# Kernel optimization log

Measured on AMD Instinct MI355X. Metric: run time of the kernel, lower is better.

Reference implementation:

```python
import jax, jax.numpy as jnp
import numpy as np
import math

N_EMBD = 512
N_BRANCH = 4
BLOCK = 2048
B, T = 2, 2048


def make_rope_tables(dim, max_len):
    inv_freq = 1.0 / (10000.0 ** (np.arange(0, dim, 2, dtype=np.float32) / dim))
    t = np.arange(max_len, dtype=np.float32)
    freqs = np.einsum('i,j->ij', t, inv_freq)  # [max_len, dim/2]
    return jnp.asarray(np.cos(freqs)), jnp.asarray(np.sin(freqs))


def apply_rope(xq, cos, sin):
    # xq: [..., T, C]; cos/sin: [T, C/2]
    x1 = xq[..., 0::2]
    x2 = xq[..., 1::2]
    y1 = x1 * cos - x2 * sin
    y2 = x1 * sin + x2 * cos
    return jnp.stack((y1, y2), axis=-1).reshape(xq.shape)


def setup_inputs() -> dict:
    key = jax.random.key(0)
    ks = jax.random.split(key, 6)
    C, NB = N_EMBD, N_BRANCH
    s = 1.0 / math.sqrt(C)
    a = jax.random.normal(ks[0], (B, T, C), jnp.float32)
    x = jax.random.normal(ks[1], (B, T, C), jnp.float32)
    Wq = jax.random.normal(ks[2], (C, C * NB), jnp.float32) * s
    Wk = jax.random.normal(ks[3], (C, C), jnp.float32) * s
    Wv = jax.random.normal(ks[4], (C, C * NB), jnp.float32) * s
    Wo = jax.random.normal(ks[5], (C, C), jnp.float32) * s
    cos, sin = make_rope_tables(C, BLOCK)
    return {"a": a, "x": x, "Wq": Wq, "Wk": Wk, "Wv": Wv, "Wo": Wo,
            "cos": cos, "sin": sin}


def reference(a, x, Wq, Wk, Wv, Wo, cos, sin):
    Bb, Tt, C = x.shape
    NB = Wq.shape[1] // C
    cos_t = cos[:Tt]
    sin_t = sin[:Tt]

    q = (a @ Wq).reshape(Bb, Tt, NB, C).transpose(0, 2, 1, 3)  # [B,NB,T,C]
    v = (a @ Wv).reshape(Bb, Tt, NB, C).transpose(0, 2, 1, 3)  # [B,NB,T,C]
    k = (x @ Wk)[:, None, :, :]                                # [B,1,T,C]

    q = apply_rope(q, cos_t, sin_t)
    k = apply_rope(k, cos_t, sin_t)

    att = jnp.einsum('bntc,bosc->bnts', q, k) / math.sqrt(C)   # [B,NB,T,T]
    causal = jnp.tril(jnp.ones((Tt, Tt), bool))                # [T,T]
    att_m = jnp.where(causal, att, -jnp.inf)

    # softmax over branch axis; mask is identical across branches, so compute
    # on unmasked logits and zero-out masked positions (== nan_to_num of
    # softmax over fully -inf columns)
    soft_probs = jnp.where(causal, jax.nn.softmax(att, axis=1), 0.0)

    max_val = jnp.max(soft_probs, axis=1, keepdims=True)
    hard_mask = jax.lax.stop_gradient((soft_probs == max_val).astype(att.dtype))
    route_mask = jax.lax.stop_gradient(hard_mask - soft_probs) + soft_probs

    att_max = jnp.max(att_m, axis=1)                           # [B,T,T]
    attn_probs = jax.nn.softmax(att_max, axis=-1)              # [B,T,T]

    combined = attn_probs[:, None, :, :] * route_mask          # [B,NB,T,T]
    y = jnp.einsum('bnts,bnsc->btc', combined, v)              # [B,T,C]
    return y @ Wo
```

## Files before the change

### kernel.cpp

```cpp
#include <hip/hip_runtime.h>
#include <math.h>


#define B_ 2
#define T_ 2048
#define C_ 512
#define NB_ 4
#define C2_ 1024

typedef unsigned short u16;
typedef unsigned char u8;
using short8 = __attribute__((ext_vector_type(8))) short;
using bf16x8 = __attribute__((ext_vector_type(8))) __bf16;
using f32x4  = __attribute__((ext_vector_type(4))) float;

__device__ __forceinline__ float bf2f(u16 u) {
  union { unsigned int i; float f; } v; v.i = ((unsigned int)u) << 16; return v.f;
}
__device__ __forceinline__ u16 f2bf(float f) {
  union { float f; unsigned int i; } v; v.f = f;
  unsigned int u = v.i;
  return (u16)((u + 0x7fffu + ((u >> 16) & 1u)) >> 16);
}
__device__ __forceinline__ f32x4 mfma16x16x32(short8 a, short8 b, f32x4 c) {
  return __builtin_amdgcn_mfma_f32_16x16x32_bf16(
      __builtin_bit_cast(bf16x8, a), __builtin_bit_cast(bf16x8, b), c, 0, 0, 0);
}
__device__ __forceinline__ void split8(const float* s, uint4& hi, uint4& lo) {
  u16 h[8], l[8];
#pragma unroll
  for (int j = 0; j < 8; ++j) {
    h[j] = f2bf(s[j]);
    l[j] = f2bf(s[j] - bf2f(h[j]));
  }
  hi.x = h[0] | ((unsigned)h[1] << 16); hi.y = h[2] | ((unsigned)h[3] << 16);
  hi.z = h[4] | ((unsigned)h[5] << 16); hi.w = h[6] | ((unsigned)h[7] << 16);
  lo.x = l[0] | ((unsigned)l[1] << 16); lo.y = l[2] | ((unsigned)l[3] << 16);
  lo.z = l[4] | ((unsigned)l[5] << 16); lo.w = l[6] | ((unsigned)l[7] << 16);
}
__device__ __forceinline__ int swz(int row) { return ((row >> 1) & 3) << 3; }

template <int MODE>
__global__ __launch_bounds__(256) void gemm_qk(const float* __restrict__ A,
                                               const float* __restrict__ W,
                                               u16* __restrict__ out,
                                               const float* __restrict__ cosT,
                                               const float* __restrict__ sinT,
                                               const int N, const int K) {
  __shared__ u16 Ah[64][32], Al[64][32];
  __shared__ u16 Bh[64][32], Bl[64][32];
  const int tid = threadIdx.x;
  const int wave = tid >> 6, lane = tid & 63;
  const int m0 = blockIdx.y << 6, n0 = blockIdx.x << 6;
  const f32x4 zero = {0.f, 0.f, 0.f, 0.f};
  f32x4 acc[4] = {zero, zero, zero, zero};
  const int srow = tid >> 2, koff = ((tid & 3) << 3) ^ swz(tid >> 2);
  const int lrow = lane & 15, lk = ((lane >> 4) << 3) ^ swz(lane & 15);
  for (int kk = 0; kk < K; kk += 32) {
    const int kg = (tid & 3) << 3;
    float av[8];
    *(float4*)(av) = *(const float4*)(&A[(size_t)(m0 + srow) * K + kk + kg]);
    *(float4*)(av + 4) =
        *(const float4*)(&A[(size_t)(m0 + srow) * K + kk + kg + 4]);
    uint4 hi, lo;
    split8(av, hi, lo);
    *(uint4*)(&Ah[srow][koff]) = hi;
    *(uint4*)(&Al[srow][koff]) = lo;
    float wv[8];
#pragma unroll
    for (int j = 0; j < 8; ++j)
      wv[j] = W[(size_t)(kk + kg + j) * N + n0 + srow];
    split8(wv, hi, lo);
    *(uint4*)(&Bh[srow][koff]) = hi;
    *(uint4*)(&Bl[srow][koff]) = lo;
    __syncthreads();
    short8 ah = *(const short8*)(&Ah[(wave << 4) + lrow][lk]);
    short8 al = *(const short8*)(&Al[(wave << 4) + lrow][lk]);
#pragma unroll
    for (int ns = 0; ns < 4; ++ns) {
      short8 bh = *(const short8*)(&Bh[(ns << 4) + lrow][lk]);
      short8 bl = *(const short8*)(&Bl[(ns << 4) + lrow][lk]);
      acc[ns] = mfma16x16x32(ah, bh, acc[ns]);
      acc[ns] = mfma16x16x32(al, bh, acc[ns]);
      acc[ns] = mfma16x16x32(ah, bl, acc[ns]);
    }
    __syncthreads();
  }
  const int r0 = m0 + (wave << 4) + ((lane >> 4) << 2);
  const int cb = n0 + (lane & 15);
#pragma unroll
  for (int ns = 0; ns < 4; ++ns) {
#pragma unroll
    for (int r = 0; r < 4; ++r) {
      const int rg = r0 + r;
      const int cg = cb + (ns << 4);
      float v = acc[ns][r];
      float pv = __shfl_xor(v, 1);
      const int t = rg & (T_ - 1);
      const int c = (MODE == 1) ? (cg & (C_ - 1)) : cg;
      const int i = c >> 1;
      const float cf = cosT[(t << 8) + i];
      const float sf = sinT[(t << 8) + i];
      float x1 = (lane & 1) ? pv : v;
      float x2 = (lane & 1) ? v : pv;
      float y = (lane & 1) ? (x1 * sf + x2 * cf) : (x1 * cf - x2 * sf);
      if (MODE == 1) y *= 0.044194173824159216f;
      const u16 hi = f2bf(y);
      const u16 lo = f2bf(y - bf2f(hi));
      size_t rowoff;
      if (MODE == 1) {
        const int b = rg >> 11, n = cg >> 9;
        rowoff = ((size_t)((b * NB_ + n) * T_ + t)) * C2_;
      } else {
        rowoff = (size_t)rg * C2_;
      }
      out[rowoff + c] = hi;
      out[rowoff + C_ + c] = lo;
    }
  }
}

template <int AF32, int OF32>
__global__ __launch_bounds__(256) void gemm_hi(const void* __restrict__ Ap,
                                               const float* __restrict__ W,
                                               void* __restrict__ outp,
                                               const int N, const int K) {
  __shared__ u16 As[64][32];
  __shared__ u16 Bs[64][32];
  const int tid = threadIdx.x;
  const int wave = tid >> 6, lane = tid & 63;
  const int m0 = blockIdx.y << 6, n0 = blockIdx.x << 6;
  const f32x4 zero = {0.f, 0.f, 0.f, 0.f};
  f32x4 acc[4] = {zero, zero, zero, zero};
  const int srow = tid >> 2, koff = ((tid & 3) << 3) ^ swz(tid >> 2);
  const int lrow = lane & 15, lk = ((lane >> 4) << 3) ^ swz(lane & 15);
  for (int kk = 0; kk < K; kk += 32) {
    const int kg = (tid & 3) << 3;
    if (AF32) {
      const float* A = (const float*)Ap;
      float av[8];
      *(float4*)(av) = *(const float4*)(&A[(size_t)(m0 + srow) * K + kk + kg]);
      *(float4*)(av + 4) =
          *(const float4*)(&A[(size_t)(m0 + srow) * K + kk + kg + 4]);
      uint4 hi;
      hi.x = f2bf(av[0]) | ((unsigned)f2bf(av[1]) << 16);
      hi.y = f2bf(av[2]) | ((unsigned)f2bf(av[3]) << 16);
      hi.z = f2bf(av[4]) | ((unsigned)f2bf(av[5]) << 16);
      hi.w = f2bf(av[6]) | ((unsigned)f2bf(av[7]) << 16);
      *(uint4*)(&As[srow][koff]) = hi;
    } else {
      const u16* A = (const u16*)Ap;
      *(uint4*)(&As[srow][koff]) =
          *(const uint4*)(&A[(size_t)(m0 + srow) * K + kk + kg]);
    }
    uint4 hi;
    {
      float w[8];
#pragma unroll
      for (int j = 0; j < 8; ++j)
        w[j] = W[(size_t)(kk + kg + j) * N + n0 + srow];
      hi.x = f2bf(w[0]) | ((unsigned)f2bf(w[1]) << 16);
      hi.y = f2bf(w[2]) | ((unsigned)f2bf(w[3]) << 16);
      hi.z = f2bf(w[4]) | ((unsigned)f2bf(w[5]) << 16);
      hi.w = f2bf(w[6]) | ((unsigned)f2bf(w[7]) << 16);
    }
    *(uint4*)(&Bs[srow][koff]) = hi;
    __syncthreads();
    short8 af = *(const short8*)(&As[(wave << 4) + lrow][lk]);
#pragma unroll
    for (int ns = 0; ns < 4; ++ns) {
      short8 bf = *(const short8*)(&Bs[(ns << 4) + lrow][lk]);
      acc[ns] = mfma16x16x32(af, bf, acc[ns]);
    }
    __syncthreads();
  }
  const int r0 = m0 + (wave << 4) + ((lane >> 4) << 2);
  const int cb = n0 + (lane & 15);
#pragma unroll
  for (int ns = 0; ns < 4; ++ns) {
#pragma unroll
    for (int r = 0; r < 4; ++r) {
      const size_t idx = (size_t)(r0 + r) * N + cb + (ns << 4);
      if (OF32) ((float*)outp)[idx] = acc[ns][r];
      else ((u16*)outp)[idx] = f2bf(acc[ns][r]);
    }
  }
}

__global__ __launch_bounds__(256) void transpose_v_k(const u16* __restrict__ Vraw,
                                                     u16* __restrict__ VT) {
  const int bid = blockIdx.x;
  const int ct = bid & 7;
  const int ttile = (bid >> 3) & 31;
  const int n = (bid >> 8) & 3;
  const int b = bid >> 10;
  __shared__ u16 tile[64][68];
  const int tid = threadIdx.x;
  const int rr = tid >> 4;
  const int cc = (tid & 15) << 2;
  const int t0 = ttile << 6, c0 = ct << 6;
#pragma unroll
  for (int it = 0; it < 4; ++it) {
    const int r = (it << 4) + rr;
    *(ushort4*)(&tile[r][cc]) = *(const ushort4*)(
        &Vraw[((size_t)((b << 11) + t0 + r)) * (NB_ * C_) + n * C_ + c0 + cc]);
  }
  __syncthreads();
#pragma unroll
  for (int it = 0; it < 4; ++it) {
    const int c = (it << 4) + rr;
    ushort4 w;
    w.x = tile[cc + 0][c]; w.y = tile[cc + 1][c];
    w.z = tile[cc + 2][c]; w.w = tile[cc + 3][c];
    *(ushort4*)(&VT[((size_t)((b * NB_ + n) * C_ + c0 + c)) * T_ + t0 + cc]) = w;
  }
}

__global__ __launch_bounds__(256) void scores_k(const u16* __restrict__ Qcat,
                                                const u16* __restrict__ Kcat,
                                                u16* __restrict__ Mout,
                                                u8* __restrict__ Mask) {
  const int tri = ((blockIdx.x & 7) * 66) + (blockIdx.x >> 3);
  int tt = (int)((sqrtf(8.f * (float)tri + 1.f) - 1.f) * 0.5f);
  while ((tt + 1) * (tt + 2) / 2 <= tri) ++tt;
  while (tt * (tt + 1) / 2 > tri) --tt;
  const int ss = tri - tt * (tt + 1) / 2;
  const int b = blockIdx.y;
  __shared__ u16 Qh[NB_][64][32], Ql[NB_][64][32];
  __shared__ u16 Kh[64][32], Kl[64][32];
  const int tid = threadIdx.x;
  const int wave = tid >> 6, lane = tid & 63;
  const int t0 = tt << 6, s0 = ss << 6;
  const f32x4 zero = {0.f, 0.f, 0.f, 0.f};
  f32x4 acc[NB_][4];
  for (int n = 0; n < NB_; ++n)
    for (int j = 0; j < 4; ++j) acc[n][j] = zero;
  const int srow = tid >> 2, koff = ((tid & 3) << 3) ^ swz(tid >> 2);
  const int lrow = lane & 15, lk = ((lane >> 4) << 3) ^ swz(lane & 15);
  const int kg = (tid & 3) << 3;
  for (int kk = 0; kk < C_; kk += 32) {
#pragma unroll
    for (int n = 0; n < NB_; ++n) {
      const size_t qb =
          ((size_t)((b * NB_ + n) * T_ + t0 + srow)) * C2_ + kk + kg;
      *(uint4*)(&Qh[n][srow][koff]) = *(const uint4*)(&Qcat[qb]);
      *(uint4*)(&Ql[n][srow][koff]) = *(const uint4*)(&Qcat[qb + C_]);
    }
    const size_t kb = ((size_t)((b << 11) + s0 + srow)) * C2_ + kk + kg;
    *(uint4*)(&Kh[srow][koff]) = *(const uint4*)(&Kcat[kb]);
    *(uint4*)(&Kl[srow][koff]) = *(const uint4*)(&Kcat[kb + C_]);
    __syncthreads();
    short8 qh[NB_], ql[NB_];
#pragma unroll
    for (int n = 0; n < NB_; ++n) {
      qh[n] = *(const short8*)(&Qh[n][(wave << 4) + lrow][lk]);
      ql[n] = *(const short8*)(&Ql[n][(wave << 4) + lrow][lk]);
    }
#pragma unroll
    for (int ns = 0; ns < 4; ++ns) {
      short8 kh = *(const short8*)(&Kh[(ns << 4) + lrow][lk]);
      short8 kl = *(const short8*)(&Kl[(ns << 4) + lrow][lk]);
#pragma unroll
      for (int n = 0; n < NB_; ++n) {
        acc[n][ns] = mfma16x16x32(qh[n], kh, acc[n][ns]);
        acc[n][ns] = mfma16x16x32(ql[n], kh, acc[n][ns]);
        acc[n][ns] = mfma16x16x32(qh[n], kl, acc[n][ns]);
      }
    }
    __syncthreads();
  }
  const int tb = t0 + (wave << 4) + ((lane >> 4) << 2);
  const int sb = s0 + (lane & 15);
#pragma unroll
  for (int ns = 0; ns < 4; ++ns) {
#pragma unroll
    for (int r = 0; r < 4; ++r) {
      const int t = tb + r, s = sb + (ns << 4);
      float a0 = acc[0][ns][r], a1 = acc[1][ns][r];
      float a2 = acc[2][ns][r], a3 = acc[3][ns][r];
      float m = fmaxf(fmaxf(a0, a1), fmaxf(a2, a3));
      u8 msk = (u8)((a0 == m) | ((a1 == m) << 1) | ((a2 == m) << 2) |
                    ((a3 == m) << 3));
      if (s > t) { m = -__builtin_inff(); msk = 0; }
      const size_t idx = (size_t)b * T_ * T_ + (size_t)t * T_ + s;
      Mout[idx] = f2bf(m);
      Mask[idx] = msk;
    }
  }
}

__global__ __launch_bounds__(256) void rowstats_k(const u16* __restrict__ Mb,
                                                  float* __restrict__ Rm,
                                                  float* __restrict__ Rz) {
  const int r = (blockIdx.x << 2) + (threadIdx.x >> 6);
  const int lane = threadIdx.x & 63;
  const int b = r >> 11, t = r & (T_ - 1);
  const u16* row = Mb + (size_t)b * T_ * T_ + (size_t)t * T_;
  float m = -__builtin_inff();
  for (int s = lane; s <= t; s += 64) m = fmaxf(m, bf2f(row[s]));
#pragma unroll
  for (int off = 32; off; off >>= 1) m = fmaxf(m, __shfl_xor(m, off));
  float z = 0.f;
  for (int s = lane; s <= t; s += 64) z += __expf(bf2f(row[s]) - m);
#pragma unroll
  for (int off = 32; off; off >>= 1) z += __shfl_xor(z, off);
  if (lane == 0) { Rm[r] = m; Rz[r] = 1.f / z; }
}

__global__ __launch_bounds__(256) void pv_k(const u16* __restrict__ Mb,
                                            const float* __restrict__ Rm,
                                            const float* __restrict__ Rz,
                                            const u8* __restrict__ Mask,
                                            const u16* __restrict__ VT,
                                            u16* __restrict__ Y) {
  const int ypair = blockIdx.x, cblk = blockIdx.y, b = blockIdx.z;
  const int c0 = cblk << 5;
  __shared__ u16 Ps[NB_][64][32];
  __shared__ u16 Vs[NB_][32][32];
  const int tid = threadIdx.x;
  const int wave = tid >> 6, lane = tid & 63;
  const int prow = tid >> 2, soff = (tid & 3) << 3;
  const int psoff = soff ^ swz(prow);
  const int vrow = tid >> 3, vsoff = (tid & 7) << 2;
  const int vcol = ((((tid & 7) >> 1) ^ ((vrow >> 1) & 3)) << 3) |
                   ((tid & 1) << 2);
  const int lrow = lane & 15, lk = ((lane >> 4) << 3) ^ swz(lane & 15);
  const f32x4 zero = {0.f, 0.f, 0.f, 0.f};
  const size_t vrow_base[NB_] = {
      ((size_t)((b * NB_ + 0) * C_ + c0 + vrow)) * T_,
      ((size_t)((b * NB_ + 1) * C_ + c0 + vrow)) * T_,
      ((size_t)((b * NB_ + 2) * C_ + c0 + vrow)) * T_,
      ((size_t)((b * NB_ + 3) * C_ + c0 + vrow)) * T_};

  for (int half = 0; half < 2; ++half) {
    const int tt = half ? (31 - ypair) : ypair;
    const int t0 = tt << 6;
    const int nchunk = (tt + 1) << 1;
    const int rg = (b << 11) + t0 + prow;
    const size_t pro = (size_t)rg << 11;
    const float rm = Rm[rg], rz = Rz[rg];
    f32x4 acc[2] = {zero, zero};
    uint4 pu; uint2 mk2; uint2 vv[NB_];
    pu = *(const uint4*)(&Mb[pro + soff]);
    mk2 = *(const uint2*)(&Mask[pro + soff]);
#pragma unroll
    for (int n = 0; n < NB_; ++n)
      vv[n] = *(const uint2*)(&VT[vrow_base[n] + vsoff]);
    for (int ck = 0; ck < nchunk; ++ck) {
      u16 m8[8] = {(u16)pu.x, (u16)(pu.x >> 16), (u16)pu.y, (u16)(pu.y >> 16),
                   (u16)pu.z, (u16)(pu.z >> 16), (u16)pu.w, (u16)(pu.w >> 16)};
      u16 p[8];
#pragma unroll
      for (int j = 0; j < 8; ++j)
        p[j] = f2bf(__expf(bf2f(m8[j]) - rm) * rz);
      u8 mk[8] = {(u8)mk2.x, (u8)(mk2.x >> 8), (u8)(mk2.x >> 16),
                  (u8)(mk2.x >> 24), (u8)mk2.y, (u8)(mk2.y >> 8),
                  (u8)(mk2.y >> 16), (u8)(mk2.y >> 24)};
#pragma unroll
      for (int n = 0; n < NB_; ++n) {
        uint4 wv;
        wv.x = (unsigned)(((mk[0] >> n) & 1) ? p[0] : 0) |
               ((unsigned)(((mk[1] >> n) & 1) ? p[1] : 0) << 16);
        wv.y = (unsigned)(((mk[2] >> n) & 1) ? p[2] : 0) |
               ((unsigned)(((mk[3] >> n) & 1) ? p[3] : 0) << 16);
        wv.z = (unsigned)(((mk[4] >> n) & 1) ? p[4] : 0) |
               ((unsigned)(((mk[5] >> n) & 1) ? p[5] : 0) << 16);
        wv.w = (unsigned)(((mk[6] >> n) & 1) ? p[6] : 0) |
               ((unsigned)(((mk[7] >> n) & 1) ? p[7] : 0) << 16);
        *(uint4*)(&Ps[n][prow][psoff]) = wv;
        *(uint2*)(&Vs[n][vrow][vcol]) = vv[n];
      }
      __syncthreads();
      if (ck + 1 < nchunk) {
        const int sB = (ck + 1) << 5;
        pu = *(const uint4*)(&Mb[pro + sB + soff]);
        mk2 = *(const uint2*)(&Mask[pro + sB + soff]);
#pragma unroll
        for (int n = 0; n < NB_; ++n)
          vv[n] = *(const uint2*)(&VT[vrow_base[n] + sB + vsoff]);
      }
#pragma unroll
      for (int n = 0; n < NB_; ++n) {
        short8 af = *(const short8*)(&Ps[n][(wave << 4) + lrow][lk]);
#pragma unroll
        for (int cs = 0; cs < 2; ++cs) {
          short8 bf = *(const short8*)(&Vs[n][(cs << 4) + lrow][lk]);
          acc[cs] = mfma16x16x32(af, bf, acc[cs]);
        }
      }
      __syncthreads();
    }
    const int tb = t0 + (wave << 4) + ((lane >> 4) << 2);
    const int cbs = c0 + (lane & 15);
#pragma unroll
    for (int cs = 0; cs < 2; ++cs) {
#pragma unroll
      for (int r = 0; r < 4; ++r) {
        Y[(size_t)((b << 11) + tb + r) * C_ + cbs + (cs << 4)] =
            f2bf(acc[cs][r]);
      }
    }
  }
}

extern "C" void kernel_launch(void* const* d_in, const int* in_sizes, int n_in,
                              void* d_out, int out_size, void* d_ws,
                              size_t ws_size, hipStream_t stream) {
  (void)in_sizes; (void)n_in; (void)out_size; (void)ws_size;
  const float* a    = (const float*)d_in[0];
  const float* x    = (const float*)d_in[1];
  const float* Wq   = (const float*)d_in[2];
  const float* Wk   = (const float*)d_in[3];
  const float* Wv   = (const float*)d_in[4];
  const float* Wo   = (const float*)d_in[5];
  const float* cosT = (const float*)d_in[6];
  const float* sinT = (const float*)d_in[7];

  char* w = (char*)d_ws;
  u16* Qcat   = (u16*)(w + 0);
  u16* Kcat   = (u16*)(w + 33554432);
  u16* Vraw   = (u16*)(w + 41943040);
  u16* VT     = (u16*)(w + 58720256);
  u8*  Mask   = (u8*)(w + 75497472);
  float* Rm   = (float*)(w + 83886080);
  float* Rz   = (float*)(w + 83902464);
  u16* Mb     = Vraw;
  u16* Y      = Qcat;

  const dim3 blk(256);
  gemm_qk<1><<<dim3(32, 64), blk, 0, stream>>>(a, Wq, Qcat, cosT, sinT, 2048, 512);
  gemm_qk<2><<<dim3(8, 64), blk, 0, stream>>>(x, Wk, Kcat, cosT, sinT, 512, 512);
  gemm_hi<1, 0><<<dim3(32, 64), blk, 0, stream>>>(a, Wv, (void*)Vraw, 2048, 512);
  transpose_v_k<<<dim3(2048), blk, 0, stream>>>(Vraw, VT);
  scores_k<<<dim3(528, 2), blk, 0, stream>>>(Qcat, Kcat, Mb, Mask);
  rowstats_k<<<dim3(1024), blk, 0, stream>>>(Mb, Rm, Rz);
  pv_k<<<dim3(16, 16, 2), blk, 0, stream>>>(Mb, Rm, Rz, Mask, VT, Y);
  gemm_hi<0, 1><<<dim3(8, 64), blk, 0, stream>>>(Y, Wo, d_out, 512, 512);
}
```

Measured before the change: 371.0 us.

## Widen PV tile to 64 output columns with 512-thread blocks

The probability-times-V kernel now computes a 64-column output tile per block using 8 waves instead of 32 columns with 4 waves, halving the grid's column dimension. Each P tile (exp, normalize, mask) is therefore computed and staged once for twice as many output columns, which halves the redundant exponentials and P reads across blocks. In exchange, blocks are larger with fewer total blocks, which may reduce occupancy and load balance, and the shared-memory layout and swizzle are reworked.

```diff
diff --git a/kernel.cpp b/kernel.cpp
--- a/kernel.cpp
+++ b/kernel.cpp
@@ -307,91 +307,83 @@
   if (lane == 0) { Rm[r] = m; Rz[r] = 1.f / z; }
 }
 
-__global__ __launch_bounds__(256) void pv_k(const u16* __restrict__ Mb,
+__global__ __launch_bounds__(512) void pv_k(const u16* __restrict__ Mb,
                                             const float* __restrict__ Rm,
                                             const float* __restrict__ Rz,
                                             const u8* __restrict__ Mask,
                                             const u16* __restrict__ VT,
                                             u16* __restrict__ Y) {
   const int ypair = blockIdx.x, cblk = blockIdx.y, b = blockIdx.z;
-  const int c0 = cblk << 5;
+  const int c0 = cblk << 6;
   __shared__ u16 Ps[NB_][64][32];
-  __shared__ u16 Vs[NB_][32][32];
+  __shared__ u16 Vs[NB_][64][32];
   const int tid = threadIdx.x;
   const int wave = tid >> 6, lane = tid & 63;
-  const int prow = tid >> 2, soff = (tid & 3) << 3;
-  const int psoff = soff ^ swz(prow);
-  const int vrow = tid >> 3, vsoff = (tid & 7) << 2;
-  const int vcol = ((((tid & 7) >> 1) ^ ((vrow >> 1) & 3)) << 3) |
-                   ((tid & 1) << 2);
+  const int wq = wave & 3, ch = wave >> 2;
+  const int row8 = tid >> 3, off4 = (tid & 7) << 2;
+  const int scol = off4 ^ swz(row8);
   const int lrow = lane & 15, lk = ((lane >> 4) << 3) ^ swz(lane & 15);
   const f32x4 zero = {0.f, 0.f, 0.f, 0.f};
   const size_t vrow_base[NB_] = {
-      ((size_t)((b * NB_ + 0) * C_ + c0 + vrow)) * T_,
-      ((size_t)((b * NB_ + 1) * C_ + c0 + vrow)) * T_,
-      ((size_t)((b * NB_ + 2) * C_ + c0 + vrow)) * T_,
-      ((size_t)((b * NB_ + 3) * C_ + c0 + vrow)) * T_};
+      ((size_t)((b * NB_ + 0) * C_ + c0 + row8)) * T_,
+      ((size_t)((b * NB_ + 1) * C_ + c0 + row8)) * T_,
+      ((size_t)((b * NB_ + 2) * C_ + c0 + row8)) * T_,
+      ((size_t)((b * NB_ + 3) * C_ + c0 + row8)) * T_};
 
   for (int half = 0; half < 2; ++half) {
     const int tt = half ? (31 - ypair) : ypair;
     const int t0 = tt << 6;
     const int nchunk = (tt + 1) << 1;
-    const int rg = (b << 11) + t0 + prow;
+    const int rg = (b << 11) + t0 + row8;
     const size_t pro = (size_t)rg << 11;
     const float rm = Rm[rg], rz = Rz[rg];
     f32x4 acc[2] = {zero, zero};
-    uint4 pu; uint2 mk2; uint2 vv[NB_];
-    pu = *(const uint4*)(&Mb[pro + soff]);
-    mk2 = *(const uint2*)(&Mask[pro + soff]);
+    uint2 pu; unsigned mk1; uint2 vv[NB_];
+    pu = *(const uint2*)(&Mb[pro + off4]);
+    mk1 = *(const unsigned*)(&Mask[pro + off4]);
 #pragma unroll
     for (int n = 0; n < NB_; ++n)
-      vv[n] = *(const uint2*)(&VT[vrow_base[n] + vsoff]);
+      vv[n] = *(const uint2*)(&VT[vrow_base[n] + off4]);
     for (int ck = 0; ck < nchunk; ++ck) {
-      u16 m8[8] = {(u16)pu.x, (u16)(pu.x >> 16), (u16)pu.y, (u16)(pu.y >> 16),
-                   (u16)pu.z, (u16)(pu.z >> 16), (u16)pu.w, (u16)(pu.w >> 16)};
-      u16 p[8];
-#pragma unroll
-      for (int j = 0; j < 8; ++j)
-        p[j] = f2bf(__expf(bf2f(m8[j]) - rm) * rz);
-      u8 mk[8] = {(u8)mk2.x, (u8)(mk2.x >> 8), (u8)(mk2.x >> 16),
-                  (u8)(mk2.x >> 24), (u8)mk2.y, (u8)(mk2.y >> 8),
-                  (u8)(mk2.y >> 16), (u8)(mk2.y >> 24)};
+      u16 m4[4] = {(u16)pu.x, (u16)(pu.x >> 16), (u16)pu.y, (u16)(pu.y >> 16)};
+      u16 p[4];
+#pragma unroll
+      for (int j = 0; j < 4; ++j)
+        p[j] = f2bf(__expf(bf2f(m4[j]) - rm) * rz);
+      u8 mk[4] = {(u8)mk1, (u8)(mk1 >> 8), (u8)(mk1 >> 16), (u8)(mk1 >> 24)};
 #pragma unroll
       for (int n = 0; n < NB_; ++n) {
-        uint4 wv;
+        uint2 wv;
         wv.x = (unsigned)(((mk[0] >> n) & 1) ? p[0] : 0) |
                ((unsigned)(((mk[1] >> n) & 1) ? p[1] : 0) << 16);
         wv.y = (unsigned)(((mk[2] >> n) & 1) ? p[2] : 0) |
                ((unsigned)(((mk[3] >> n) & 1) ? p[3] : 0) << 16);
-        wv.z = (unsigned)(((mk[4] >> n) & 1) ? p[4] : 0) |
-               ((unsigned)(((mk[5] >> n) & 1) ? p[5] : 0) << 16);
-        wv.w = (unsigned)(((mk[6] >> n) & 1) ? p[6] : 0) |
-               ((unsigned)(((mk[7] >> n) & 1) ? p[7] : 0) << 16);
-        *(uint4*)(&Ps[n][prow][psoff]) = wv;
-        *(uint2*)(&Vs[n][vrow][vcol]) = vv[n];
+        *(uint2*)(&Ps[n][row8][scol]) = wv;
+        *(uint2*)(&Vs[n][row8][scol]) = vv[n];
       }
       __syncthreads();
       if (ck + 1 < nchunk) {
         const int sB = (ck + 1) << 5;
-        pu = *(const uint4*)(&Mb[pro + sB + soff]);
-        mk2 = *(const uint2*)(&Mask[pro + sB + soff]);
+        pu = *(const uint2*)(&Mb[pro + sB + off4]);
+        mk1 = *(const unsigned*)(&Mask[pro + sB + off4]);
 #pragma unroll
         for (int n = 0; n < NB_; ++n)
-          vv[n] = *(const uint2*)(&VT[vrow_base[n] + sB + vsoff]);
+          vv[n] = *(const uint2*)(&VT[vrow_base[n] + sB + off4]);
       }
 #pragma unroll
       for (int n = 0; n < NB_; ++n) {
-        short8 af = *(const short8*)(&Ps[n][(wave << 4) + lrow][lk]);
+        short8 af = *(const short8*)(&Ps[n][(wq << 4) + lrow][lk]);
 #pragma unroll
         for (int cs = 0; cs < 2; ++cs) {
-          short8 bf = *(const short8*)(&Vs[n][(cs << 4) + lrow][lk]);
+          short8 bf =
+              *(const short8*)(&Vs[n][(ch << 5) + (cs << 4) + lrow][lk]);
           acc[cs] = mfma16x16x32(af, bf, acc[cs]);
         }
       }
       __syncthreads();
     }
-    const int tb = t0 + (wave << 4) + ((lane >> 4) << 2);
-    const int cbs = c0 + (lane & 15);
+    const int tb = t0 + (wq << 4) + ((lane >> 4) << 2);
+    const int cbs = c0 + (ch << 5) + (lane & 15);
 #pragma unroll
     for (int cs = 0; cs < 2; ++cs) {
 #pragma unroll
@@ -434,6 +426,6 @@
   transpose_v_k<<<dim3(2048), blk, 0, stream>>>(Vraw, VT);
   scores_k<<<dim3(528, 2), blk, 0, stream>>>(Qcat, Kcat, Mb, Mask);
   rowstats_k<<<dim3(1024), blk, 0, stream>>>(Mb, Rm, Rz);
-  pv_k<<<dim3(16, 16, 2), blk, 0, stream>>>(Mb, Rm, Rz, Mask, VT, Y);
+  pv_k<<<dim3(16, 8, 2), dim3(512), 0, stream>>>(Mb, Rm, Rz, Mask, VT, Y);
   gemm_hi<0, 1><<<dim3(8, 64), blk, 0, stream>>>(Y, Wo, d_out, 512, 512);
 }
```

Measured after the change: 364.7 us. About the same (-1.7%).
